# Optimization experiments

Measured on AMD Instinct MI355X. Metric: run time of the kernel, lower is better.

## Reference

```python
import jax, jax.numpy as jnp
import numpy as np

DEPTH, DIM, HEADS, DH = 2, 1024, 16, 64
B, N, MEM, TEXT = 8, 256, 4, 64
PH, PW, PS = 4, 4, 16
EXP_H, EXP_W, EXP_T = 4, 4, 2
RH, RW, RT = 2*EXP_H+1, 2*EXP_W+1, 2*EXP_T+1  # 9,9,5
CUR_IDX = 20
MEM_IDXS = [0, 5, 10, 15]
SCALE = DH ** -0.5


def _pos(idx):
    # get_pos_from_idx_down_right
    nf = PH * PW
    inner = idx % nf
    return inner % PH, inner // PH, idx // nf


def _axial_freqs():
    # 2D axial rotary freqs over the (PH*PS)x(PW*PS) pixel grid, rot_dim = DH
    GH, GW = PH * PS, PW * PS
    nfa = DH // 4  # 16 base freqs per axis -> 32 dims per axis after pair-repeat
    inv = 1.0 / (10000.0 ** (np.arange(nfa, dtype=np.float64) / nfa))
    fh = np.repeat(np.arange(GH)[:, None] * inv[None, :], 2, axis=-1)  # [GH,32]
    fw = np.repeat(np.arange(GW)[:, None] * inv[None, :], 2, axis=-1)  # [GW,32]
    return np.concatenate([
        np.broadcast_to(fh[:, None, :], (GH, GW, DH // 2)),
        np.broadcast_to(fw[None, :, :], (GH, GW, DH // 2)),
    ], axis=-1).astype(np.float32)  # [GH,GW,DH]


def setup_inputs() -> dict:
    key = jax.random.key(0)
    ks = jax.random.split(key, 14)
    p = lambda k, shape: jax.random.normal(k, shape, jnp.float32) * 0.02
    x = jax.random.normal(ks[0], (B, N, DIM), jnp.float32)
    cond = jax.random.normal(ks[1], (B, MEM * N + TEXT, DIM), jnp.float32)
    Wq = p(ks[2], (DEPTH, DIM, HEADS * DH))
    Wk = p(ks[3], (DEPTH, DIM, HEADS * DH))
    Wv = p(ks[4], (DEPTH, DIM, HEADS * DH))
    Wo = p(ks[5], (DEPTH, HEADS * DH, DIM))
    bo = jnp.zeros((DEPTH, DIM), jnp.float32)
    rpe = p(ks[6], (DEPTH, RH * RW * RT, HEADS))
    W1 = p(ks[7], (DEPTH, DIM, DIM * 4 * 2))
    b1 = jnp.zeros((DEPTH, DIM * 8), jnp.float32)
    W2 = p(ks[8], (DEPTH, DIM * 4, DIM))
    b2 = jnp.zeros((DEPTH, DIM), jnp.float32)
    freqs = _axial_freqs()
    def block(idx):
        r, c, _ = _pos(idx)
        return freqs[r * PS:(r + 1) * PS, c * PS:(c + 1) * PS].reshape(-1, DH)
    src_freq = jnp.asarray(block(CUR_IDX))
    tgt_freq = jnp.asarray(np.concatenate([block(i) for i in MEM_IDXS], axis=0))
    sr, sc, st = _pos(CUR_IDX)
    rel = [(tr - sr + EXP_H) * RW + (tc - sc + EXP_W) + (tt - st + EXP_T) * RH * RW
           for (tr, tc, tt) in map(_pos, MEM_IDXS)]
    rel_idx = jnp.asarray(rel, jnp.int32)
    return dict(x=x, cond=cond, Wq=Wq, Wk=Wk, Wv=Wv, Wo=Wo, bo=bo, rpe=rpe,
                W1=W1, b1=b1, W2=W2, b2=b2, src_freq=src_freq, tgt_freq=tgt_freq,
                rel_idx=rel_idx)


def _rotate_half(t):
    # pairs interleaved: (d r) with r=2
    tr = t.reshape(t.shape[:-1] + (-1, 2))
    t1, t2 = tr[..., 0], tr[..., 1]
    return jnp.stack((-t2, t1), axis=-1).reshape(t.shape)


def _apply_rotary(freqs, t):
    return t * jnp.cos(freqs) + _rotate_half(t) * jnp.sin(freqs)


def reference(x, cond, Wq, Wk, Wv, Wo, bo, rpe, W1, b1, W2, b2, src_freq, tgt_freq, rel_idx):
    MS = MEM * N  # memory token count in cond
    split_heads = lambda t: t.reshape(t.shape[0], t.shape[1], HEADS, DH).transpose(0, 2, 1, 3)
    for l in range(DEPTH):
        # --- FullCrossAttention ---
        q = split_heads(x @ Wq[l])          # [b,h,n,dh]
        k = split_heads(cond @ Wk[l])       # [b,h,j,dh]
        v = split_heads(cond @ Wv[l])
        # gathered relative-position bias added to k (broadcast over feature dim)
        bias = rpe[l][rel_idx]              # [mem, h]
        bias_k = jnp.repeat(bias.T, N, axis=1)[None, :, :, None]  # [1,h,mem*S,1]
        k = k.at[:, :, :MS, :].add(bias_k)
        # inline rotary: src freqs on q, gathered target freqs on memory keys
        q = _apply_rotary(src_freq, q)
        k = k.at[:, :, :MS, :].set(_apply_rotary(tgt_freq, k[:, :, :MS, :]))
        dots = jnp.einsum('bhid,bhjd->bhij', q, k) * SCALE
        attn = jax.nn.softmax(dots, axis=-1)
        out = jnp.einsum('bhij,bhjd->bhid', attn, v)
        out = out.transpose(0, 2, 1, 3).reshape(x.shape[0], N, HEADS * DH)
        x = x + out @ Wo[l] + bo[l]
        # --- GEGLU FeedForward ---
        hgl = x @ W1[l] + b1[l]
        a, g = jnp.split(hgl, 2, axis=-1)
        y = a * jax.nn.gelu(g, approximate=False)
        x = x + y @ W2[l] + b2[l]
    return x
```

## Files before the change

kernel.cpp:

```cpp
#include <hip/hip_runtime.h>
#include <hip/hip_bf16.h>
#include <math.h>

typedef __hip_bfloat16 bf16;
typedef __bf16 bf16x8 __attribute__((ext_vector_type(8)));
typedef float f32x4 __attribute__((ext_vector_type(4)));

typedef __attribute__((address_space(3))) void lds_void;
typedef const __attribute__((address_space(1))) void gbl_void;

__device__ __forceinline__ float b2f(bf16 v) { return __bfloat162float(v); }
__device__ __forceinline__ bf16 f2b(float v) { return __float2bfloat16(v); }

__device__ __forceinline__ f32x4 shfl_xor4(f32x4 v, int m) {
  f32x4 o;
  o[0] = __shfl_xor(v[0], m);
  o[1] = __shfl_xor(v[1], m);
  o[2] = __shfl_xor(v[2], m);
  o[3] = __shfl_xor(v[3], m);
  return o;
}
__device__ __forceinline__ f32x4 max4(f32x4 a, f32x4 b) {
  f32x4 o;
  o[0] = fmaxf(a[0], b[0]); o[1] = fmaxf(a[1], b[1]);
  o[2] = fmaxf(a[2], b[2]); o[3] = fmaxf(a[3], b[3]);
  return o;
}
__device__ __forceinline__ f32x4 exp4(f32x4 a) {
  f32x4 o;
  o[0] = __expf(a[0]); o[1] = __expf(a[1]);
  o[2] = __expf(a[2]); o[3] = __expf(a[3]);
  return o;
}

__global__ void detect_dtype(const unsigned int* __restrict__ x, int* __restrict__ flag) {
  int cnt = 0;
  for (int i = 0; i < 128; ++i) {
    unsigned int lo = x[i] & 0xFFFFu;
    unsigned int e = (lo >> 7) & 0xFFu;
    if (e >= 100u && e <= 140u) ++cnt;
  }
  *flag = (cnt >= 96) ? 1 : 0;
}

__global__ void convert_in(const void* __restrict__ src, bf16* __restrict__ dst,
                           int n, const int* __restrict__ flag) {
  int i = blockIdx.x * 256 + threadIdx.x;
  if (i >= n) return;
  dst[i] = (*flag) ? ((const bf16*)src)[i] : f2b(((const float*)src)[i]);
}

__global__ void emit_kernel(const float* __restrict__ xf, const int* __restrict__ flag,
                            void* __restrict__ out) {
  int i = blockIdx.x * 256 + threadIdx.x;
  if (*flag) ((bf16*)out)[i] = f2b(xf[i]);
  else       ((float*)out)[i] = xf[i];
}

template<int TAG>
__global__ __launch_bounds__(256, 2) void gemm_bt(
    const bf16* __restrict__ A, int lda,
    const bf16* __restrict__ Bt, int ldb,
    float alpha,
    const float* __restrict__ resid,
    const bf16* __restrict__ bias,
    float* __restrict__ outf,
    bf16* __restrict__ outb,
    int ldc, int K)
{
  __shared__ char smem[65536] __attribute__((aligned(16)));
  float* lC = (float*)smem;

  int tid = threadIdx.x;
  int lane = tid & 63;
  int wave = tid >> 6;
  int quad = lane >> 4, l16 = lane & 15;
  int wm = (wave >> 1) * 64, wn = (wave & 1) * 64;
  int row0 = blockIdx.y * 128, col0 = blockIdx.x * 128;

  const bf16* asrc[4]; const bf16* bsrc[4];
#pragma unroll
  for (int i = 0; i < 4; ++i) {
    int row = i * 32 + (tid >> 3);
    int coff = ((tid & 7) * 16) ^ ((row & 7) << 4);
    asrc[i] = A + (long long)(row0 + row) * lda + (coff >> 1);
    bsrc[i] = Bt + (long long)(col0 + row) * ldb + (coff >> 1);
  }
  int ldsbase = wave * 1024;

  f32x4 acc[4][4];
#pragma unroll
  for (int a = 0; a < 4; ++a)
#pragma unroll
    for (int b = 0; b < 4; ++b) acc[a][b] = (f32x4){0.f, 0.f, 0.f, 0.f};

  int nk = K >> 6;
#pragma unroll
  for (int i = 0; i < 4; ++i) {
    __builtin_amdgcn_global_load_lds((gbl_void*)(asrc[i]),
        (lds_void*)(smem + i * 4096 + ldsbase), 16, 0, 0);
    __builtin_amdgcn_global_load_lds((gbl_void*)(bsrc[i]),
        (lds_void*)(smem + 16384 + i * 4096 + ldsbase), 16, 0, 0);
  }
  __syncthreads();

  for (int t = 0; t < nk; ++t) {
    int buf = (t & 1) << 15;
    int nbuf = buf ^ 32768;
    if (t + 1 < nk) {
      int k0 = (t + 1) << 6;
#pragma unroll
      for (int i = 0; i < 4; ++i) {
        __builtin_amdgcn_global_load_lds((gbl_void*)(asrc[i] + k0),
            (lds_void*)(smem + nbuf + i * 4096 + ldsbase), 16, 0, 0);
        __builtin_amdgcn_global_load_lds((gbl_void*)(bsrc[i] + k0),
            (lds_void*)(smem + nbuf + 16384 + i * 4096 + ldsbase), 16, 0, 0);
      }
    }
    const __bf16* lA = (const __bf16*)(smem + buf);
    const __bf16* lB = (const __bf16*)(smem + buf + 16384);
#pragma unroll
    for (int ks = 0; ks < 2; ++ks) {
      bf16x8 af[4], bfr[4];
#pragma unroll
      for (int mi = 0; mi < 4; ++mi) {
        int r = wm + mi * 16 + l16;
        af[mi] = *(const bf16x8*)&lA[r * 64 + ((ks * 32 + quad * 8) ^ ((r & 7) << 3))];
      }
#pragma unroll
      for (int ni = 0; ni < 4; ++ni) {
        int r = wn + ni * 16 + l16;
        bfr[ni] = *(const bf16x8*)&lB[r * 64 + ((ks * 32 + quad * 8) ^ ((r & 7) << 3))];
      }
      __builtin_amdgcn_s_setprio(1);
#pragma unroll
      for (int mi = 0; mi < 4; ++mi)
#pragma unroll
        for (int ni = 0; ni < 4; ++ni)
          acc[mi][ni] = __builtin_amdgcn_mfma_f32_16x16x32_bf16(
              af[mi], bfr[ni], acc[mi][ni], 0, 0, 0);
      __builtin_amdgcn_s_setprio(0);
    }
    __syncthreads();
  }

#pragma unroll
  for (int half = 0; half < 2; ++half) {
    __syncthreads();
    if ((wave >> 1) == half) {
#pragma unroll
      for (int mi = 0; mi < 4; ++mi)
#pragma unroll
        for (int ni = 0; ni < 4; ++ni)
#pragma unroll
          for (int r = 0; r < 4; ++r)
            lC[(mi * 16 + quad * 4 + r) * 128 + wn + ni * 16 + l16] =
                acc[mi][ni][r] * alpha;
    }
    __syncthreads();
#pragma unroll
    for (int i = 0; i < 8; ++i) {
      int f = i * 256 + tid;
      int row = f >> 5, cc = (f & 31) * 4;
      int m = row0 + half * 64 + row, n = col0 + cc;
      f32x4 v = *(const f32x4*)&lC[row * 128 + cc];
      long long ci = (long long)m * ldc + n;
      if (bias) {
        v[0] += b2f(bias[n]);     v[1] += b2f(bias[n + 1]);
        v[2] += b2f(bias[n + 2]); v[3] += b2f(bias[n + 3]);
      }
      if (resid) v += *(const f32x4*)&resid[ci];
      if (outf) *(f32x4*)&outf[ci] = v;
      if (outb) {
        bf16 c0 = f2b(v[0]), c1 = f2b(v[1]), c2 = f2b(v[2]), c3 = f2b(v[3]);
        ushort4 o = { *(unsigned short*)&c0, *(unsigned short*)&c1,
                      *(unsigned short*)&c2, *(unsigned short*)&c3 };
        *(ushort4*)&outb[ci] = o;
      }
    }
  }
}

__global__ __launch_bounds__(512, 2) void gemm256(
    const bf16* __restrict__ A, int lda,
    const bf16* __restrict__ Bt, int ldb,
    const bf16* __restrict__ bias,
    bf16* __restrict__ outb,
    int ldc, int K)
{
  __shared__ char smem[131072] __attribute__((aligned(16)));
  float* lC = (float*)smem;

  int tid = threadIdx.x;
  int lane = tid & 63;
  int wave = tid >> 6;
  int quad = lane >> 4, l16 = lane & 15;
  int wr = wave >> 2, wc = wave & 3;
  int wm = wr * 128, wn = wc * 64;
  int row0 = blockIdx.y * 256, col0 = blockIdx.x * 256;

  const bf16* asrc[4]; const bf16* bsrc[4];
#pragma unroll
  for (int i = 0; i < 4; ++i) {
    int row = i * 64 + (tid >> 3);
    int coff = ((tid & 7) * 16) ^ ((row & 7) << 4);
    asrc[i] = A + (long long)(row0 + row) * lda + (coff >> 1);
    bsrc[i] = Bt + (long long)(col0 + row) * ldb + (coff >> 1);
  }
  int ldsbase = wave * 1024;

  f32x4 acc[8][4];
#pragma unroll
  for (int a = 0; a < 8; ++a)
#pragma unroll
    for (int b = 0; b < 4; ++b) acc[a][b] = (f32x4){0.f, 0.f, 0.f, 0.f};

  int nk = K >> 6;
#pragma unroll
  for (int i = 0; i < 4; ++i) {
    __builtin_amdgcn_global_load_lds((gbl_void*)(asrc[i]),
        (lds_void*)(smem + i * 8192 + ldsbase), 16, 0, 0);
    __builtin_amdgcn_global_load_lds((gbl_void*)(bsrc[i]),
        (lds_void*)(smem + 32768 + i * 8192 + ldsbase), 16, 0, 0);
  }
  __syncthreads();

  for (int t = 0; t < nk; ++t) {
    int buf = (t & 1) << 16;
    int nbuf = buf ^ 65536;
    if (t + 1 < nk) {
      int k0 = (t + 1) << 6;
#pragma unroll
      for (int i = 0; i < 4; ++i) {
        __builtin_amdgcn_global_load_lds((gbl_void*)(asrc[i] + k0),
            (lds_void*)(smem + nbuf + i * 8192 + ldsbase), 16, 0, 0);
        __builtin_amdgcn_global_load_lds((gbl_void*)(bsrc[i] + k0),
            (lds_void*)(smem + nbuf + 32768 + i * 8192 + ldsbase), 16, 0, 0);
      }
    }
    const __bf16* lA = (const __bf16*)(smem + buf);
    const __bf16* lB = (const __bf16*)(smem + buf + 32768);
#pragma unroll
    for (int ks = 0; ks < 2; ++ks) {
      bf16x8 af[8], bfr[4];
#pragma unroll
      for (int mi = 0; mi < 8; ++mi) {
        int r = wm + mi * 16 + l16;
        af[mi] = *(const bf16x8*)&lA[r * 64 + ((ks * 32 + quad * 8) ^ ((r & 7) << 3))];
      }
#pragma unroll
      for (int ni = 0; ni < 4; ++ni) {
        int r = wn + ni * 16 + l16;
        bfr[ni] = *(const bf16x8*)&lB[r * 64 + ((ks * 32 + quad * 8) ^ ((r & 7) << 3))];
      }
      __builtin_amdgcn_s_setprio(1);
#pragma unroll
      for (int mi = 0; mi < 8; ++mi)
#pragma unroll
        for (int ni = 0; ni < 4; ++ni)
          acc[mi][ni] = __builtin_amdgcn_mfma_f32_16x16x32_bf16(
              af[mi], bfr[ni], acc[mi][ni], 0, 0, 0);
      __builtin_amdgcn_s_setprio(0);
    }
    __syncthreads();
  }

#pragma unroll
  for (int h = 0; h < 2; ++h) {
    __syncthreads();
    if (wr == h) {
#pragma unroll
      for (int mi = 0; mi < 8; ++mi)
#pragma unroll
        for (int ni = 0; ni < 4; ++ni)
#pragma unroll
          for (int r = 0; r < 4; ++r)
            lC[(mi * 16 + quad * 4 + r) * 256 + wn + ni * 16 + l16] =
                acc[mi][ni][r];
    }
    __syncthreads();
#pragma unroll
    for (int it = 0; it < 16; ++it) {
      int f = it * 512 + tid;
      int row = f >> 6, cc = (f & 63) * 4;
      int m = row0 + h * 128 + row, n = col0 + cc;
      f32x4 v = *(const f32x4*)&lC[row * 256 + cc];
      v[0] += b2f(bias[n]);     v[1] += b2f(bias[n + 1]);
      v[2] += b2f(bias[n + 2]); v[3] += b2f(bias[n + 3]);
      bf16 c0 = f2b(v[0]), c1 = f2b(v[1]), c2 = f2b(v[2]), c3 = f2b(v[3]);
      ushort4 o = { *(unsigned short*)&c0, *(unsigned short*)&c1,
                    *(unsigned short*)&c2, *(unsigned short*)&c3 };
      *(ushort4*)&outb[(long long)m * ldc + n] = o;
    }
  }
}

__global__ __launch_bounds__(256, 2) void gemm_splitk(
    const bf16* __restrict__ A, int lda,
    const bf16* __restrict__ Bt, int ldb,
    float* __restrict__ pbuf, int ldc, int M, int KC)
{
  __shared__ char smem[65536] __attribute__((aligned(16)));

  int koff = blockIdx.z * KC;
  float* outz = pbuf + (long long)blockIdx.z * M * ldc;
  int tid = threadIdx.x;
  int lane = tid & 63;
  int wave = tid >> 6;
  int quad = lane >> 4, l16 = lane & 15;
  int wm = (wave >> 1) * 64, wn = (wave & 1) * 64;
  int row0 = blockIdx.y * 128, col0 = blockIdx.x * 128;

  const bf16* asrc[4]; const bf16* bsrc[4];
#pragma unroll
  for (int i = 0; i < 4; ++i) {
    int row = i * 32 + (tid >> 3);
    int coff = ((tid & 7) * 16) ^ ((row & 7) << 4);
    asrc[i] = A + (long long)(row0 + row) * lda + koff + (coff >> 1);
    bsrc[i] = Bt + (long long)(col0 + row) * ldb + koff + (coff >> 1);
  }
  int ldsbase = wave * 1024;

  f32x4 acc[4][4];
#pragma unroll
  for (int a = 0; a < 4; ++a)
#pragma unroll
    for (int b = 0; b < 4; ++b) acc[a][b] = (f32x4){0.f, 0.f, 0.f, 0.f};

  int nk = KC >> 6;
#pragma unroll
  for (int i = 0; i < 4; ++i) {
    __builtin_amdgcn_global_load_lds((gbl_void*)(asrc[i]),
        (lds_void*)(smem + i * 4096 + ldsbase), 16, 0, 0);
    __builtin_amdgcn_global_load_lds((gbl_void*)(bsrc[i]),
        (lds_void*)(smem + 16384 + i * 4096 + ldsbase), 16, 0, 0);
  }
  __syncthreads();

  for (int t = 0; t < nk; ++t) {
    int buf = (t & 1) << 15;
    int nbuf = buf ^ 32768;
    if (t + 1 < nk) {
      int k0 = (t + 1) << 6;
#pragma unroll
      for (int i = 0; i < 4; ++i) {
        __builtin_amdgcn_global_load_lds((gbl_void*)(asrc[i] + k0),
            (lds_void*)(smem + nbuf + i * 4096 + ldsbase), 16, 0, 0);
        __builtin_amdgcn_global_load_lds((gbl_void*)(bsrc[i] + k0),
            (lds_void*)(smem + nbuf + 16384 + i * 4096 + ldsbase), 16, 0, 0);
      }
    }
    const __bf16* lA = (const __bf16*)(smem + buf);
    const __bf16* lB = (const __bf16*)(smem + buf + 16384);
#pragma unroll
    for (int ks = 0; ks < 2; ++ks) {
      bf16x8 af[4], bfr[4];
#pragma unroll
      for (int mi = 0; mi < 4; ++mi) {
        int r = wm + mi * 16 + l16;
        af[mi] = *(const bf16x8*)&lA[r * 64 + ((ks * 32 + quad * 8) ^ ((r & 7) << 3))];
      }
#pragma unroll
      for (int ni = 0; ni < 4; ++ni) {
        int r = wn + ni * 16 + l16;
        bfr[ni] = *(const bf16x8*)&lB[r * 64 + ((ks * 32 + quad * 8) ^ ((r & 7) << 3))];
      }
      __builtin_amdgcn_s_setprio(1);
#pragma unroll
      for (int mi = 0; mi < 4; ++mi)
#pragma unroll
        for (int ni = 0; ni < 4; ++ni)
          acc[mi][ni] = __builtin_amdgcn_mfma_f32_16x16x32_bf16(
              af[mi], bfr[ni], acc[mi][ni], 0, 0, 0);
      __builtin_amdgcn_s_setprio(0);
    }
    __syncthreads();
  }

#pragma unroll
  for (int mi = 0; mi < 4; ++mi)
#pragma unroll
    for (int ni = 0; ni < 4; ++ni) {
      int n = col0 + wn + ni * 16 + l16;
#pragma unroll
      for (int r = 0; r < 4; ++r) {
        int m = row0 + wm + mi * 16 + quad * 4 + r;
        outz[(long long)m * ldc + n] = acc[mi][ni][r];
      }
    }
}

__global__ void reduce_ff2(const float* __restrict__ pbuf, const bf16* __restrict__ bias,
                           float* __restrict__ xf, bf16* __restrict__ xbf) {
  int i = blockIdx.x * 256 + threadIdx.x;
  const int NT = 2048 * 1024;
  float v = xf[i] + b2f(bias[i & 1023]) +
            pbuf[i] + pbuf[i + NT] + pbuf[i + 2 * NT] + pbuf[i + 3 * NT];
  xf[i] = v;
  xbf[i] = f2b(v);
}

template<int TK>
__device__ __forceinline__ void fa_tile(
    const bf16* __restrict__ kb, const bf16* __restrict__ vtb, int j0,
    const bf16x8 (&qa)[2][2], __bf16* lK, __bf16* lV, bf16* lPw,
    int tid, int quad, int l16,
    f32x4 (&accO)[2][4], f32x4 (&mrow)[2], f32x4 (&lrow)[2])
{
  constexpr int NT = TK / 16;
  constexpr int NCH = TK / 32;
  __syncthreads();
#pragma unroll
  for (int i = 0; i < TK / 32; ++i) {
    int t = i * 256 + tid;
    int r = t >> 3, c = (t & 7) * 8;
    *(uint4*)&lK[r * 72 + c] = *(const uint4*)&kb[(long long)(j0 + r) * 1024 + c];
  }
#pragma unroll
  for (int i = 0; i < TK / 32; ++i) {
    int t = i * 256 + tid;
    int d = t / (TK / 8), c = (t % (TK / 8)) * 8;
    *(uint4*)&lV[d * 136 + c] = *(const uint4*)&vtb[(long long)d * 8704 + j0 + c];
  }
  __syncthreads();

  f32x4 accS[2][NT];
#pragma unroll
  for (int mi = 0; mi < 2; ++mi)
#pragma unroll
    for (int ni = 0; ni < NT; ++ni) accS[mi][ni] = (f32x4){0.f, 0.f, 0.f, 0.f};

#pragma unroll
  for (int ni = 0; ni < NT; ++ni)
#pragma unroll
    for (int ks = 0; ks < 2; ++ks) {
      bf16x8 bfr = *(const bf16x8*)&lK[(ni * 16 + l16) * 72 + ks * 32 + quad * 8];
      accS[0][ni] = __builtin_amdgcn_mfma_f32_16x16x32_bf16(qa[0][ks], bfr, accS[0][ni], 0, 0, 0);
      accS[1][ni] = __builtin_amdgcn_mfma_f32_16x16x32_bf16(qa[1][ks], bfr, accS[1][ni], 0, 0, 0);
    }

#pragma unroll
  for (int mi = 0; mi < 2; ++mi) {
    f32x4 vmax = (f32x4){-INFINITY, -INFINITY, -INFINITY, -INFINITY};
#pragma unroll
    for (int ni = 0; ni < NT; ++ni) {
      accS[mi][ni] *= 0.125f;
      vmax = max4(vmax, accS[mi][ni]);
    }
#pragma unroll
    for (int m = 1; m <= 8; m <<= 1) vmax = max4(vmax, shfl_xor4(vmax, m));
    f32x4 mnew = max4(mrow[mi], vmax);
    f32x4 alpha = exp4(mrow[mi] - mnew);
    f32x4 rs = (f32x4){0.f, 0.f, 0.f, 0.f};
#pragma unroll
    for (int ni = 0; ni < NT; ++ni) {
      accS[mi][ni] = exp4(accS[mi][ni] - mnew);
      rs += accS[mi][ni];
    }
#pragma unroll
    for (int m = 1; m <= 8; m <<= 1) rs += shfl_xor4(rs, m);
    lrow[mi] = lrow[mi] * alpha + rs;
    mrow[mi] = mnew;
#pragma unroll
    for (int nd = 0; nd < 4; ++nd) accO[mi][nd] *= alpha;
  }

#pragma unroll
  for (int c = 0; c < NCH; ++c) {
#pragma unroll
    for (int mi = 0; mi < 2; ++mi)
#pragma unroll
      for (int u = 0; u < 2; ++u) {
#pragma unroll
        for (int r = 0; r < 4; ++r)
          lPw[(mi * 16 + quad * 4 + r) * 40 + u * 16 + l16] = f2b(accS[mi][c * 2 + u][r]);
      }
#pragma unroll
    for (int nd = 0; nd < 4; ++nd) {
      bf16x8 vb = *(const bf16x8*)&lV[(nd * 16 + l16) * 136 + c * 32 + quad * 8];
      bf16x8 pa0 = *(const bf16x8*)&lPw[(l16) * 40 + quad * 8];
      bf16x8 pa1 = *(const bf16x8*)&lPw[(16 + l16) * 40 + quad * 8];
      accO[0][nd] = __builtin_amdgcn_mfma_f32_16x16x32_bf16(pa0, vb, accO[0][nd], 0, 0, 0);
      accO[1][nd] = __builtin_amdgcn_mfma_f32_16x16x32_bf16(pa1, vb, accO[1][nd], 0, 0, 0);
    }
  }
}

__global__ __launch_bounds__(256, 1) void flash_attn(
    const bf16* __restrict__ q, const bf16* __restrict__ k,
    const bf16* __restrict__ vt, bf16* __restrict__ att)
{
  __shared__ __bf16 lK[128 * 72] __attribute__((aligned(16)));
  __shared__ __bf16 lV[64 * 136] __attribute__((aligned(16)));
  __shared__ __bf16 lP[4][32 * 40] __attribute__((aligned(16)));

  int idx = blockIdx.x;
  int b = idx >> 5, h = (idx >> 1) & 15, half = idx & 1;
  int tid = threadIdx.x, wave = tid >> 6, lane = tid & 63;
  int quad = lane >> 4, l16 = lane & 15;
  int qrow0 = b * 256 + half * 128 + wave * 32;

  const bf16* kb  = k  + (long long)b * 1088 * 1024 + h * 64;
  const bf16* vtb = vt + (long long)(h * 64) * 8704 + b * 1088;
  bf16* lPw = (bf16*)&lP[wave][0];

  bf16x8 qa[2][2];
#pragma unroll
  for (int mi = 0; mi < 2; ++mi)
#pragma unroll
    for (int ks = 0; ks < 2; ++ks)
      qa[mi][ks] = *(const bf16x8*)&q[(long long)(qrow0 + mi * 16 + l16) * 1024 +
                                      h * 64 + ks * 32 + quad * 8];

  f32x4 accO[2][4];
  f32x4 mrow[2], lrow[2];
#pragma unroll
  for (int mi = 0; mi < 2; ++mi) {
    mrow[mi] = (f32x4){-INFINITY, -INFINITY, -INFINITY, -INFINITY};
    lrow[mi] = (f32x4){0.f, 0.f, 0.f, 0.f};
#pragma unroll
    for (int nd = 0; nd < 4; ++nd) accO[mi][nd] = (f32x4){0.f, 0.f, 0.f, 0.f};
  }

  for (int jt = 0; jt < 8; ++jt)
    fa_tile<128>(kb, vtb, jt * 128, qa, lK, lV, lPw, tid, quad, l16, accO, mrow, lrow);
  fa_tile<64>(kb, vtb, 1024, qa, lK, lV, lPw, tid, quad, l16, accO, mrow, lrow);

#pragma unroll
  for (int mi = 0; mi < 2; ++mi) {
    f32x4 inv;
    inv[0] = 1.f / lrow[mi][0]; inv[1] = 1.f / lrow[mi][1];
    inv[2] = 1.f / lrow[mi][2]; inv[3] = 1.f / lrow[mi][3];
#pragma unroll
    for (int nd = 0; nd < 4; ++nd) {
      f32x4 o = accO[mi][nd] * inv;
#pragma unroll
      for (int r = 0; r < 4; ++r)
        att[(long long)(qrow0 + mi * 16 + quad * 4 + r) * 1024 +
            h * 64 + nd * 16 + l16] = f2b(o[r]);
    }
  }
}

__global__ void init_x_kernel(const void* __restrict__ x, const int* __restrict__ flag,
                              float* __restrict__ xf, bf16* __restrict__ xbf) {
  int i = blockIdx.x * 256 + threadIdx.x;
  float v = (*flag) ? b2f(((const bf16*)x)[i]) : ((const float*)x)[i];
  xf[i] = v;
  xbf[i] = f2b(v);
}

__global__ void transpose_w(const void* __restrict__ in, bf16* __restrict__ out,
                            int R, int C, const int* __restrict__ flag) {
  __shared__ bf16 tile[32][33];
  long long zoff = (long long)blockIdx.z * R * C;
  const bf16* inb = (const bf16*)in + zoff;
  const float* inf = (const float*)in + zoff;
  out += zoff;
  int tx = threadIdx.x, ty = threadIdx.y;
  int c0 = blockIdx.x * 32, r0 = blockIdx.y * 32;
  int isb = *flag;
#pragma unroll
  for (int i = 0; i < 4; ++i) {
    long long off = (long long)(r0 + ty + i * 8) * C + (c0 + tx);
    tile[ty + i * 8][tx] = isb ? inb[off] : f2b(inf[off]);
  }
  __syncthreads();
#pragma unroll
  for (int i = 0; i < 4; ++i)
    out[(long long)(c0 + ty + i * 8) * R + (r0 + tx)] = tile[tx][ty + i * 8];
}

__global__ void rotary_q_kernel(bf16* __restrict__ q, const bf16* __restrict__ srcf) {
  int idx = blockIdx.x * 256 + threadIdx.x;
  int row = idx >> 9;
  int p = idx & 511;
  int h = p >> 5, i = p & 31;
  int d0 = h * 64 + 2 * i;
  int ntok = row & 255;
  float f = b2f(srcf[ntok * 64 + 2 * i]);
  float c = cosf(f), s = sinf(f);
  long long base = (long long)row * 1024 + d0;
  float q0 = b2f(q[base]), q1 = b2f(q[base + 1]);
  q[base]     = f2b(q0 * c - q1 * s);
  q[base + 1] = f2b(q1 * c + q0 * s);
}

__global__ void k_bias_rot_kernel(bf16* __restrict__ k, const bf16* __restrict__ tgtf,
                                  const bf16* __restrict__ rpe,
                                  const int* __restrict__ ridx, int layer) {
  int idx = blockIdx.x * 256 + threadIdx.x;
  int b = idx >> 19;
  int rem = idx & ((1 << 19) - 1);
  int j = rem >> 9;
  int p = rem & 511;
  int h = p >> 5, i = p & 31;
  int d0 = h * 64 + 2 * i;
  float bias = b2f(rpe[(layer * 405 + ridx[j >> 8]) * 16 + h]);
  float f = b2f(tgtf[j * 64 + 2 * i]);
  float c = cosf(f), s = sinf(f);
  long long base = (long long)(b * 1088 + j) * 1024 + d0;
  float k0 = b2f(k[base]) + bias, k1 = b2f(k[base + 1]) + bias;
  k[base]     = f2b(k0 * c - k1 * s);
  k[base + 1] = f2b(k1 * c + k0 * s);
}

__global__ void geglu_kernel(const bf16* __restrict__ hgl, bf16* __restrict__ y) {
  int idx = blockIdx.x * 256 + threadIdx.x;
  int m = idx >> 12, n = idx & 4095;
  float a = b2f(hgl[(long long)m * 8192 + n]);
  float g = b2f(hgl[(long long)m * 8192 + 4096 + n]);
  float ge = 0.5f * g * (1.0f + erff(g * 0.70710678118654752f));
  y[idx] = f2b(a * ge);
}

extern "C" void kernel_launch(void* const* d_in, const int* in_sizes, int n_in,
                              void* d_out, int out_size, void* d_ws, size_t ws_size,
                              hipStream_t stream) {
  (void)in_sizes; (void)n_in; (void)out_size; (void)ws_size;
  const void* x    = d_in[0];
  const void* cond = d_in[1];
  const void* Wq   = d_in[2];
  const void* Wk   = d_in[3];
  const void* Wv   = d_in[4];
  const void* Wo   = d_in[5];
  const void* bo   = d_in[6];
  const void* rpe  = d_in[7];
  const void* W1   = d_in[8];
  const void* b1   = d_in[9];
  const void* W2   = d_in[10];
  const void* b2   = d_in[11];
  const void* srcf = d_in[12];
  const void* tgtf = d_in[13];
  const int*  ridx = (const int*)d_in[14];

  char* w = (char*)d_ws;
  int* flag = (int*)w;   w += 256;
  bf16* WqT = (bf16*)w;  w += (size_t)2 * 1024 * 1024 * 2;
  bf16* WkT = (bf16*)w;  w += (size_t)2 * 1024 * 1024 * 2;
  bf16* WvT = (bf16*)w;  w += (size_t)2 * 1024 * 1024 * 2;
  bf16* WoT = (bf16*)w;  w += (size_t)2 * 1024 * 1024 * 2;
  bf16* W1T = (bf16*)w;  w += (size_t)2 * 8192 * 1024 * 2;
  bf16* W2T = (bf16*)w;  w += (size_t)2 * 4096 * 1024 * 2;
  bf16* condb = (bf16*)w; w += (size_t)8704 * 1024 * 2;
  bf16* bo_b = (bf16*)w;  w += 2048 * 2;
  bf16* rpe_b = (bf16*)w; w += 12960 * 2;
  bf16* b1_b = (bf16*)w;  w += 16384 * 2;
  bf16* b2_b = (bf16*)w;  w += 2048 * 2;
  bf16* srcf_b = (bf16*)w; w += 16384 * 2;
  bf16* tgtf_b = (bf16*)w; w += 65536 * 2;
  float* xf = (float*)w; w += (size_t)2048 * 1024 * 4;
  bf16* xbf = (bf16*)w;  w += (size_t)2048 * 1024 * 2;
  bf16* qbuf = (bf16*)w; w += (size_t)2048 * 1024 * 2;
  bf16* kbuf = (bf16*)w; w += (size_t)8704 * 1024 * 2;
  bf16* vTf = (bf16*)w;  w += (size_t)1024 * 8704 * 2;
  bf16* att = (bf16*)w;  w += (size_t)2048 * 1024 * 2;
  bf16* hgl = (bf16*)w;  w += (size_t)2048 * 8192 * 2;
  bf16* ybuf = (bf16*)w; w += (size_t)2048 * 4096 * 2;
  float* pbuf = (float*)hgl;

  detect_dtype<<<1, 1, 0, stream>>>((const unsigned int*)x, flag);

  convert_in<<<34816, 256, 0, stream>>>(cond, condb, 8704 * 1024, flag);
  convert_in<<<8, 256, 0, stream>>>(bo, bo_b, 2048, flag);
  convert_in<<<51, 256, 0, stream>>>(rpe, rpe_b, 12960, flag);
  convert_in<<<64, 256, 0, stream>>>(b1, b1_b, 16384, flag);
  convert_in<<<8, 256, 0, stream>>>(b2, b2_b, 2048, flag);
  convert_in<<<64, 256, 0, stream>>>(srcf, srcf_b, 16384, flag);
  convert_in<<<256, 256, 0, stream>>>(tgtf, tgtf_b, 65536, flag);

  dim3 tb(32, 8);
  transpose_w<<<dim3(32, 32, 2),  tb, 0, stream>>>(Wq, WqT, 1024, 1024, flag);
  transpose_w<<<dim3(32, 32, 2),  tb, 0, stream>>>(Wk, WkT, 1024, 1024, flag);
  transpose_w<<<dim3(32, 32, 2),  tb, 0, stream>>>(Wv, WvT, 1024, 1024, flag);
  transpose_w<<<dim3(32, 32, 2),  tb, 0, stream>>>(Wo, WoT, 1024, 1024, flag);
  transpose_w<<<dim3(256, 32, 2), tb, 0, stream>>>(W1, W1T, 1024, 8192, flag);
  transpose_w<<<dim3(32, 128, 2), tb, 0, stream>>>(W2, W2T, 4096, 1024, flag);
  init_x_kernel<<<8192, 256, 0, stream>>>(x, flag, xf, xbf);

  for (int l = 0; l < 2; ++l) {
    const bf16* WqTl = WqT + (size_t)l * 1024 * 1024;
    const bf16* WkTl = WkT + (size_t)l * 1024 * 1024;
    const bf16* WvTl = WvT + (size_t)l * 1024 * 1024;
    const bf16* WoTl = WoT + (size_t)l * 1024 * 1024;
    const bf16* W1Tl = W1T + (size_t)l * 8192 * 1024;
    const bf16* W2Tl = W2T + (size_t)l * 4096 * 1024;

    gemm_bt<0><<<dim3(8, 16), 256, 0, stream>>>(xbf, 1024, WqTl, 1024, 1.f,
        nullptr, nullptr, nullptr, qbuf, 1024, 1024);
    rotary_q_kernel<<<4096, 256, 0, stream>>>(qbuf, srcf_b);
    gemm_bt<1><<<dim3(68, 8), 256, 0, stream>>>(WvTl, 1024, condb, 1024, 1.f,
        nullptr, nullptr, nullptr, vTf, 8704, 1024);
    gemm_bt<2><<<dim3(8, 68), 256, 0, stream>>>(condb, 1024, WkTl, 1024, 1.f,
        nullptr, nullptr, nullptr, kbuf, 1024, 1024);
    k_bias_rot_kernel<<<16384, 256, 0, stream>>>(kbuf, tgtf_b, rpe_b, ridx, l);
    flash_attn<<<256, 256, 0, stream>>>(qbuf, kbuf, vTf, att);
    gemm_bt<3><<<dim3(8, 16), 256, 0, stream>>>(att, 1024, WoTl, 1024, 1.f,
        xf, bo_b + (size_t)l * 1024, xf, xbf, 1024, 1024);
    gemm256<<<dim3(32, 8), 512, 0, stream>>>(xbf, 1024, W1Tl, 1024,
        b1_b + (size_t)l * 8192, hgl, 8192, 1024);
    geglu_kernel<<<32768, 256, 0, stream>>>(hgl, ybuf);
    gemm_splitk<<<dim3(8, 16, 4), 256, 0, stream>>>(ybuf, 4096, W2Tl, 4096,
                                                    pbuf, 1024, 2048, 1024);
    reduce_ff2<<<8192, 256, 0, stream>>>(pbuf, b2_b + (size_t)l * 1024, xf, xbf);
  }

  emit_kernel<<<8192, 256, 0, stream>>>(xf, flag, d_out);
}
```

Before: 826.7 us.

## Double-buffer flash attention K/V tiles via direct global-to-LDS loads with swizzle

Reworks the flash attention kernel to use 512 threads (8 waves of 16 query rows each) instead of 4 waves of 32 rows. K and V tiles are loaded with global_load_lds directly into XOR-swizzled LDS buffers, double-buffered so the next tile's load overlaps the current tile's compute. This hides global latency and removes the padded LDS layout and register staging, at the cost of more LDS (~74KB) and less per-wave query reuse of K/V fragments.

```diff
diff --git a/kernel.cpp b/kernel.cpp
--- a/kernel.cpp
+++ b/kernel.cpp
@@ -400,145 +400,141 @@
   xbf[i] = f2b(v);
 }
 
+__device__ __forceinline__ void fa_stage(
+    const bf16* __restrict__ kb, const bf16* __restrict__ vtb, int j0, int tk,
+    char* smem, int kboff, int vboff, int tid, int wave)
+{
+  int rounds = tk >> 6;
+  for (int i = 0; i < rounds; ++i) {
+    int rowk = i * 64 + (tid >> 3);
+    int cbk = ((tid & 7) * 16) ^ ((rowk & 7) << 4);
+    __builtin_amdgcn_global_load_lds(
+        (gbl_void*)(kb + (long long)(j0 + rowk) * 1024 + (cbk >> 1)),
+        (lds_void*)(smem + kboff + i * 8192 + wave * 1024), 16, 0, 0);
+    int rowv, cbv;
+    if (tk == 128) { rowv = i * 32 + (tid >> 4); cbv = ((tid & 15) * 16) ^ ((rowv & 7) << 4); }
+    else           { rowv = (tid >> 3);          cbv = ((tid & 7) * 16) ^ ((rowv & 7) << 4); }
+    __builtin_amdgcn_global_load_lds(
+        (gbl_void*)(vtb + (long long)rowv * 8704 + j0 + (cbv >> 1)),
+        (lds_void*)(smem + vboff + i * 8192 + wave * 1024), 16, 0, 0);
+  }
+}
+
 template<int TK>
-__device__ __forceinline__ void fa_tile(
-    const bf16* __restrict__ kb, const bf16* __restrict__ vtb, int j0,
-    const bf16x8 (&qa)[2][2], __bf16* lK, __bf16* lV, bf16* lPw,
-    int tid, int quad, int l16,
-    f32x4 (&accO)[2][4], f32x4 (&mrow)[2], f32x4 (&lrow)[2])
+__device__ __forceinline__ void fa_compute(
+    const char* smem, int kboff, int vboff,
+    const bf16x8 (&qa)[2], bf16* lPw,
+    int quad, int l16,
+    f32x4 (&accO)[4], f32x4& mrow, f32x4& lrow)
 {
   constexpr int NT = TK / 16;
   constexpr int NCH = TK / 32;
-  __syncthreads();
-#pragma unroll
-  for (int i = 0; i < TK / 32; ++i) {
-    int t = i * 256 + tid;
-    int r = t >> 3, c = (t & 7) * 8;
-    *(uint4*)&lK[r * 72 + c] = *(const uint4*)&kb[(long long)(j0 + r) * 1024 + c];
-  }
-#pragma unroll
-  for (int i = 0; i < TK / 32; ++i) {
-    int t = i * 256 + tid;
-    int d = t / (TK / 8), c = (t % (TK / 8)) * 8;
-    *(uint4*)&lV[d * 136 + c] = *(const uint4*)&vtb[(long long)d * 8704 + j0 + c];
-  }
-  __syncthreads();
-
-  f32x4 accS[2][NT];
-#pragma unroll
-  for (int mi = 0; mi < 2; ++mi)
-#pragma unroll
-    for (int ni = 0; ni < NT; ++ni) accS[mi][ni] = (f32x4){0.f, 0.f, 0.f, 0.f};
+  const __bf16* lK = (const __bf16*)(smem + kboff);
+  const __bf16* lV = (const __bf16*)(smem + vboff);
+  int xork = (l16 & 7) << 3;
+
+  f32x4 accS[NT];
+#pragma unroll
+  for (int ni = 0; ni < NT; ++ni) accS[ni] = (f32x4){0.f, 0.f, 0.f, 0.f};
 
 #pragma unroll
   for (int ni = 0; ni < NT; ++ni)
 #pragma unroll
     for (int ks = 0; ks < 2; ++ks) {
-      bf16x8 bfr = *(const bf16x8*)&lK[(ni * 16 + l16) * 72 + ks * 32 + quad * 8];
-      accS[0][ni] = __builtin_amdgcn_mfma_f32_16x16x32_bf16(qa[0][ks], bfr, accS[0][ni], 0, 0, 0);
-      accS[1][ni] = __builtin_amdgcn_mfma_f32_16x16x32_bf16(qa[1][ks], bfr, accS[1][ni], 0, 0, 0);
-    }
-
-#pragma unroll
-  for (int mi = 0; mi < 2; ++mi) {
-    f32x4 vmax = (f32x4){-INFINITY, -INFINITY, -INFINITY, -INFINITY};
-#pragma unroll
-    for (int ni = 0; ni < NT; ++ni) {
-      accS[mi][ni] *= 0.125f;
-      vmax = max4(vmax, accS[mi][ni]);
-    }
-#pragma unroll
-    for (int m = 1; m <= 8; m <<= 1) vmax = max4(vmax, shfl_xor4(vmax, m));
-    f32x4 mnew = max4(mrow[mi], vmax);
-    f32x4 alpha = exp4(mrow[mi] - mnew);
-    f32x4 rs = (f32x4){0.f, 0.f, 0.f, 0.f};
-#pragma unroll
-    for (int ni = 0; ni < NT; ++ni) {
-      accS[mi][ni] = exp4(accS[mi][ni] - mnew);
-      rs += accS[mi][ni];
-    }
-#pragma unroll
-    for (int m = 1; m <= 8; m <<= 1) rs += shfl_xor4(rs, m);
-    lrow[mi] = lrow[mi] * alpha + rs;
-    mrow[mi] = mnew;
-#pragma unroll
-    for (int nd = 0; nd < 4; ++nd) accO[mi][nd] *= alpha;
-  }
+      bf16x8 bfr = *(const bf16x8*)&lK[(ni * 16 + l16) * 64 + ((ks * 32 + quad * 8) ^ xork)];
+      accS[ni] = __builtin_amdgcn_mfma_f32_16x16x32_bf16(qa[ks], bfr, accS[ni], 0, 0, 0);
+    }
+
+  f32x4 vmax = (f32x4){-INFINITY, -INFINITY, -INFINITY, -INFINITY};
+#pragma unroll
+  for (int ni = 0; ni < NT; ++ni) {
+    accS[ni] *= 0.125f;
+    vmax = max4(vmax, accS[ni]);
+  }
+#pragma unroll
+  for (int m = 1; m <= 8; m <<= 1) vmax = max4(vmax, shfl_xor4(vmax, m));
+  f32x4 mnew = max4(mrow, vmax);
+  f32x4 alpha = exp4(mrow - mnew);
+  f32x4 rs = (f32x4){0.f, 0.f, 0.f, 0.f};
+#pragma unroll
+  for (int ni = 0; ni < NT; ++ni) {
+    accS[ni] = exp4(accS[ni] - mnew);
+    rs += accS[ni];
+  }
+#pragma unroll
+  for (int m = 1; m <= 8; m <<= 1) rs += shfl_xor4(rs, m);
+  lrow = lrow * alpha + rs;
+  mrow = mnew;
+#pragma unroll
+  for (int nd = 0; nd < 4; ++nd) accO[nd] *= alpha;
 
 #pragma unroll
   for (int c = 0; c < NCH; ++c) {
 #pragma unroll
-    for (int mi = 0; mi < 2; ++mi)
-#pragma unroll
-      for (int u = 0; u < 2; ++u) {
-#pragma unroll
-        for (int r = 0; r < 4; ++r)
-          lPw[(mi * 16 + quad * 4 + r) * 40 + u * 16 + l16] = f2b(accS[mi][c * 2 + u][r]);
-      }
+    for (int u = 0; u < 2; ++u)
+#pragma unroll
+      for (int r = 0; r < 4; ++r)
+        lPw[(quad * 4 + r) * 40 + u * 16 + l16] = f2b(accS[c * 2 + u][r]);
+    bf16x8 pa = *(const bf16x8*)&lPw[l16 * 40 + quad * 8];
 #pragma unroll
     for (int nd = 0; nd < 4; ++nd) {
-      bf16x8 vb = *(const bf16x8*)&lV[(nd * 16 + l16) * 136 + c * 32 + quad * 8];
-      bf16x8 pa0 = *(const bf16x8*)&lPw[(l16) * 40 + quad * 8];
-      bf16x8 pa1 = *(const bf16x8*)&lPw[(16 + l16) * 40 + quad * 8];
-      accO[0][nd] = __builtin_amdgcn_mfma_f32_16x16x32_bf16(pa0, vb, accO[0][nd], 0, 0, 0);
-      accO[1][nd] = __builtin_amdgcn_mfma_f32_16x16x32_bf16(pa1, vb, accO[1][nd], 0, 0, 0);
-    }
-  }
-}
-
-__global__ __launch_bounds__(256, 1) void flash_attn(
+      bf16x8 vb = *(const bf16x8*)&lV[(nd * 16 + l16) * TK + ((c * 32 + quad * 8) ^ xork)];
+      accO[nd] = __builtin_amdgcn_mfma_f32_16x16x32_bf16(pa, vb, accO[nd], 0, 0, 0);
+    }
+  }
+}
+
+__global__ __launch_bounds__(512, 2) void flash_attn(
     const bf16* __restrict__ q, const bf16* __restrict__ k,
     const bf16* __restrict__ vt, bf16* __restrict__ att)
 {
-  __shared__ __bf16 lK[128 * 72] __attribute__((aligned(16)));
-  __shared__ __bf16 lV[64 * 136] __attribute__((aligned(16)));
-  __shared__ __bf16 lP[4][32 * 40] __attribute__((aligned(16)));
+  __shared__ char smem[75776] __attribute__((aligned(16)));
 
   int idx = blockIdx.x;
   int b = idx >> 5, h = (idx >> 1) & 15, half = idx & 1;
   int tid = threadIdx.x, wave = tid >> 6, lane = tid & 63;
   int quad = lane >> 4, l16 = lane & 15;
-  int qrow0 = b * 256 + half * 128 + wave * 32;
+  int qrow0 = b * 256 + half * 128 + wave * 16;
 
   const bf16* kb  = k  + (long long)b * 1088 * 1024 + h * 64;
   const bf16* vtb = vt + (long long)(h * 64) * 8704 + b * 1088;
-  bf16* lPw = (bf16*)&lP[wave][0];
-
-  bf16x8 qa[2][2];
-#pragma unroll
-  for (int mi = 0; mi < 2; ++mi)
-#pragma unroll
-    for (int ks = 0; ks < 2; ++ks)
-      qa[mi][ks] = *(const bf16x8*)&q[(long long)(qrow0 + mi * 16 + l16) * 1024 +
-                                      h * 64 + ks * 32 + quad * 8];
-
-  f32x4 accO[2][4];
-  f32x4 mrow[2], lrow[2];
-#pragma unroll
-  for (int mi = 0; mi < 2; ++mi) {
-    mrow[mi] = (f32x4){-INFINITY, -INFINITY, -INFINITY, -INFINITY};
-    lrow[mi] = (f32x4){0.f, 0.f, 0.f, 0.f};
-#pragma unroll
-    for (int nd = 0; nd < 4; ++nd) accO[mi][nd] = (f32x4){0.f, 0.f, 0.f, 0.f};
-  }
-
-  for (int jt = 0; jt < 8; ++jt)
-    fa_tile<128>(kb, vtb, jt * 128, qa, lK, lV, lPw, tid, quad, l16, accO, mrow, lrow);
-  fa_tile<64>(kb, vtb, 1024, qa, lK, lV, lPw, tid, quad, l16, accO, mrow, lrow);
-
-#pragma unroll
-  for (int mi = 0; mi < 2; ++mi) {
-    f32x4 inv;
-    inv[0] = 1.f / lrow[mi][0]; inv[1] = 1.f / lrow[mi][1];
-    inv[2] = 1.f / lrow[mi][2]; inv[3] = 1.f / lrow[mi][3];
-#pragma unroll
-    for (int nd = 0; nd < 4; ++nd) {
-      f32x4 o = accO[mi][nd] * inv;
-#pragma unroll
-      for (int r = 0; r < 4; ++r)
-        att[(long long)(qrow0 + mi * 16 + quad * 4 + r) * 1024 +
-            h * 64 + nd * 16 + l16] = f2b(o[r]);
-    }
+  bf16* lPw = (bf16*)(smem + 65536 + wave * 1280);
+
+  bf16x8 qa[2];
+#pragma unroll
+  for (int ks = 0; ks < 2; ++ks)
+    qa[ks] = *(const bf16x8*)&q[(long long)(qrow0 + l16) * 1024 +
+                                h * 64 + ks * 32 + quad * 8];
+
+  f32x4 accO[4];
+  f32x4 mrow = (f32x4){-INFINITY, -INFINITY, -INFINITY, -INFINITY};
+  f32x4 lrow = (f32x4){0.f, 0.f, 0.f, 0.f};
+#pragma unroll
+  for (int nd = 0; nd < 4; ++nd) accO[nd] = (f32x4){0.f, 0.f, 0.f, 0.f};
+
+  fa_stage(kb, vtb, 0, 128, smem, 0, 32768, tid, wave);
+  __syncthreads();
+
+  for (int jt = 0; jt < 8; ++jt) {
+    int buf = (jt & 1) * 16384;
+    int nbuf = 16384 - buf;
+    if (jt < 7) fa_stage(kb, vtb, (jt + 1) * 128, 128, smem, nbuf, 32768 + nbuf, tid, wave);
+    else        fa_stage(kb, vtb, 1024, 64, smem, nbuf, 32768 + nbuf, tid, wave);
+    fa_compute<128>(smem, buf, 32768 + buf, qa, lPw, quad, l16, accO, mrow, lrow);
+    __syncthreads();
+  }
+  fa_compute<64>(smem, 0, 32768, qa, lPw, quad, l16, accO, mrow, lrow);
+
+  f32x4 inv;
+  inv[0] = 1.f / lrow[0]; inv[1] = 1.f / lrow[1];
+  inv[2] = 1.f / lrow[2]; inv[3] = 1.f / lrow[3];
+#pragma unroll
+  for (int nd = 0; nd < 4; ++nd) {
+    f32x4 o = accO[nd] * inv;
+#pragma unroll
+    for (int r = 0; r < 4; ++r)
+      att[(long long)(qrow0 + quad * 4 + r) * 1024 +
+          h * 64 + nd * 16 + l16] = f2b(o[r]);
   }
 }
 
@@ -694,7 +690,7 @@
     gemm_bt<2><<<dim3(8, 68), 256, 0, stream>>>(condb, 1024, WkTl, 1024, 1.f,
         nullptr, nullptr, nullptr, kbuf, 1024, 1024);
     k_bias_rot_kernel<<<16384, 256, 0, stream>>>(kbuf, tgtf_b, rpe_b, ridx, l);
-    flash_attn<<<256, 256, 0, stream>>>(qbuf, kbuf, vTf, att);
+    flash_attn<<<256, 512, 0, stream>>>(qbuf, kbuf, vTf, att);
     gemm_bt<3><<<dim3(8, 16), 256, 0, stream>>>(att, 1024, WoTl, 1024, 1.f,
         xf, bo_b + (size_t)l * 1024, xf, xbf, 1024, 1024);
     gemm256<<<dim3(32, 8), 512, 0, stream>>>(xbf, 1024, W1Tl, 1024,
```

Result: faster. 785.7 us (-5.0%).
